# Kernel tuning notes

Hardware: AMD Instinct MI355X
Metric: run time of the kernel (lower is better)

Reference implementation:

```python
import jax, jax.numpy as jnp
import numpy as np

EMB_DIM = 1024
B, T = 32, 2048
N_FLIGHTS = 30
# Action index layout (ActionEnumerator): 0=no_flight, 1=cancel, 2=no_reservation,
# 3..32 = book flight i, 33..62 = change flight i  -> n_actions = 63

def setup_inputs() -> dict:
    key = jax.random.key(0)
    k0, k1, k2, k3, k4 = jax.random.split(key, 5)
    scale = 1.0 / np.sqrt(EMB_DIM)
    return {
        "embs": jax.random.normal(k0, (B, T, EMB_DIM), dtype=jnp.float32),
        "W_status": jax.random.uniform(k1, (5, EMB_DIM), jnp.float32, -scale, scale),
        "b_status": jax.random.uniform(k2, (5,), jnp.float32, -scale, scale),
        "W_flight": jax.random.uniform(k3, (N_FLIGHTS, EMB_DIM), jnp.float32, -scale, scale),
        "b_flight": jax.random.uniform(k4, (N_FLIGHTS,), jnp.float32, -scale, scale),
    }

def reference(embs, W_status, b_status, W_flight, b_flight):
    # Two small linear heads + softmax
    status_probs = jax.nn.softmax(jnp.einsum('bte,se->bts', embs, W_status) + b_status, axis=-1)
    flight_probs = jax.nn.softmax(jnp.einsum('bte,fe->btf', embs, W_flight) + b_flight, axis=-1)
    no_flight = status_probs[:, :, 0:1]
    no_reservation = status_probs[:, :, 1:2]
    cancel = status_probs[:, :, 2:3]
    change = status_probs[:, :, 3:4]
    book = status_probs[:, :, 4:5]
    # Fused version of the 30-iteration scatter loop: one concat of outer products.
    final_probs = jnp.concatenate(
        [no_flight, cancel, no_reservation,
         book * flight_probs,     # [B,T,30] book flight i
         change * flight_probs],  # [B,T,30] change flight i
        axis=-1)  # [B, T, 63]
    return final_probs
```

## Files before the change

kernel.cpp:

```cpp
#include <hip/hip_runtime.h>
#include <math.h>


typedef __bf16 bf16x8 __attribute__((ext_vector_type(8)));
typedef float  f32x4  __attribute__((ext_vector_type(4)));

#define ROWS_PER_BLOCK 256
#define KSTEPS   32
#define HALF_KS  16

__global__ __launch_bounds__(1024, 4)
void fused_heads_kernel(const float* __restrict__ embs,
                        const float* __restrict__ W_status,
                        const float* __restrict__ b_status,
                        const float* __restrict__ W_flight,
                        const float* __restrict__ b_flight,
                        float* __restrict__ out) {
    __shared__ bf16x8 Bsh[HALF_KS * 3 * 64];

    const int tid  = threadIdx.x;
    const int lane = tid & 63;
    const int wv   = tid >> 6;
    const int n    = lane & 15;
    const int q    = lane >> 4;

    const int rowbase = blockIdx.x * ROWS_PER_BLOCK + wv * 16;
    const float* aptr = embs + (size_t)(rowbase + n) * 1024 + q * 8;

    f32x4 acc0 = {0.f, 0.f, 0.f, 0.f};
    f32x4 acc1 = {0.f, 0.f, 0.f, 0.f};
    f32x4 acc2 = {0.f, 0.f, 0.f, 0.f};

    float4 ca0 = *(const float4*)(aptr);
    float4 ca1 = *(const float4*)(aptr + 4);

    for (int half = 0; half < 2; ++half) {
        __syncthreads();

#pragma unroll
        for (int i = 0; i < 3; ++i) {
            const int d   = tid + i * 1024;
            const int L   = d & 63;
            const int ksf = d >> 6;
            const int ksl = ksf / 3;
            const int f   = ksf - ksl * 3;
            const int bn  = f * 16 + (L & 15);
            const int bk  = (half * HALF_KS + ksl) * 32 + (L >> 4) * 8;
            bf16x8 w;
#pragma unroll
            for (int j = 0; j < 8; ++j) w[j] = (__bf16)0.0f;
            if (bn < 35) {
                const float* src = (bn < 5) ? (W_status + bn * 1024 + bk)
                                            : (W_flight + (bn - 5) * 1024 + bk);
                const float4 w0 = *(const float4*)(src);
                const float4 w1 = *(const float4*)(src + 4);
                w[0] = (__bf16)w0.x; w[1] = (__bf16)w0.y;
                w[2] = (__bf16)w0.z; w[3] = (__bf16)w0.w;
                w[4] = (__bf16)w1.x; w[5] = (__bf16)w1.y;
                w[6] = (__bf16)w1.z; w[7] = (__bf16)w1.w;
            }
            Bsh[d] = w;
        }
        __syncthreads();

#pragma unroll 4
        for (int kl = 0; kl < HALF_KS; ++kl) {
            const int ks  = half * HALF_KS + kl;
            const int nks = (ks < KSTEPS - 1) ? ks + 1 : ks;
            const float4 na0 = *(const float4*)(aptr + nks * 32);
            const float4 na1 = *(const float4*)(aptr + nks * 32 + 4);

            bf16x8 af;
            af[0] = (__bf16)ca0.x; af[1] = (__bf16)ca0.y;
            af[2] = (__bf16)ca0.z; af[3] = (__bf16)ca0.w;
            af[4] = (__bf16)ca1.x; af[5] = (__bf16)ca1.y;
            af[6] = (__bf16)ca1.z; af[7] = (__bf16)ca1.w;

            const bf16x8 b0 = Bsh[(kl * 3 + 0) * 64 + lane];
            const bf16x8 b1 = Bsh[(kl * 3 + 1) * 64 + lane];
            const bf16x8 b2 = Bsh[(kl * 3 + 2) * 64 + lane];

            acc0 = __builtin_amdgcn_mfma_f32_16x16x32_bf16(af, b0, acc0, 0, 0, 0);
            acc1 = __builtin_amdgcn_mfma_f32_16x16x32_bf16(af, b1, acc1, 0, 0, 0);
            acc2 = __builtin_amdgcn_mfma_f32_16x16x32_bf16(af, b2, acc2, 0, 0, 0);

            ca0 = na0; ca1 = na1;
        }
    }

    const float bias0 = (n < 5) ? b_status[n] : b_flight[n - 5];
    const float bias1 = b_flight[n + 11];
    const float bias2 = (n < 3) ? b_flight[n + 27] : 0.0f;
    const int   gb    = lane & 48;

#pragma unroll
    for (int i = 0; i < 4; ++i) {
        const float v0 = acc0[i] + bias0;
        const float v1 = acc1[i] + bias1;
        const float v2 = (n < 3) ? (acc2[i] + bias2) : -INFINITY;

        float ms = (n < 5) ? v0 : -INFINITY;
        float mf = fmaxf((n >= 5) ? v0 : -INFINITY, fmaxf(v1, v2));
#pragma unroll
        for (int m = 1; m < 16; m <<= 1) {
            ms = fmaxf(ms, __shfl_xor(ms, m));
            mf = fmaxf(mf, __shfl_xor(mf, m));
        }

        const float es  = (n < 5)  ? __expf(v0 - ms) : 0.0f;
        const float ef0 = (n >= 5) ? __expf(v0 - mf) : 0.0f;
        const float ef1 = __expf(v1 - mf);
        const float ef2 = (n < 3)  ? __expf(v2 - mf) : 0.0f;

        float ss = es;
        float sf = ef0 + ef1 + ef2;
#pragma unroll
        for (int m = 1; m < 16; m <<= 1) {
            ss += __shfl_xor(ss, m);
            sf += __shfl_xor(sf, m);
        }
        const float invs = 1.0f / ss;
        const float invf = 1.0f / sf;

        const float book   = __shfl(es, gb + 4) * invs * invf;
        const float change = __shfl(es, gb + 3) * invs * invf;

        float* orow = out + (size_t)(rowbase + q * 4 + i) * 63;
        if (n == 0) orow[0] = es * invs;
        if (n == 2) orow[1] = es * invs;
        if (n == 1) orow[2] = es * invs;
        if (n >= 5) {
            orow[3 + (n - 5)]  = book   * ef0;
            orow[33 + (n - 5)] = change * ef0;
        }
        orow[3 + (n + 11)]  = book   * ef1;
        orow[33 + (n + 11)] = change * ef1;
        if (n < 3) {
            orow[3 + (n + 27)]  = book   * ef2;
            orow[33 + (n + 27)] = change * ef2;
        }
    }
}

extern "C" void kernel_launch(void* const* d_in, const int* in_sizes, int n_in,
                              void* d_out, int out_size, void* d_ws, size_t ws_size,
                              hipStream_t stream) {
    const float* embs     = (const float*)d_in[0];
    const float* W_status = (const float*)d_in[1];
    const float* b_status = (const float*)d_in[2];
    const float* W_flight = (const float*)d_in[3];
    const float* b_flight = (const float*)d_in[4];
    float* out = (float*)d_out;

    const int rows = in_sizes[0] / 1024;
    const int grid = rows / ROWS_PER_BLOCK;

    fused_heads_kernel<<<grid, 1024, 0, stream>>>(
        embs, W_status, b_status, W_flight, b_flight, out);
}
```

Measured before the change: 391.2 us.

## Stagger K-traversal order per wave and block, load two K-steps per iteration

Each wave now walks the K dimension in pairs of steps, starting at an offset derived from its wave id and block id, and blocks alternate which half of K they process first. The intent is to spread concurrent global reads across different address ranges and channels so they do not hit the same addresses at once. Each iteration also fetches 64 contiguous floats per lane (two K-steps), which puts more loads in flight. The costs are extra register pressure and more complex index arithmetic. A leftover dead code block is also present.

```diff
diff --git a/kernel.cpp b/kernel.cpp
--- a/kernel.cpp
+++ b/kernel.cpp
@@ -6,8 +6,9 @@
 typedef float  f32x4  __attribute__((ext_vector_type(4)));
 
 #define ROWS_PER_BLOCK 256
-#define KSTEPS   32
-#define HALF_KS  16
+#define KSTEPS    32
+#define HALF_KS   16
+#define HALF_PAIRS 8
 
 __global__ __launch_bounds__(1024, 4)
 void fused_heads_kernel(const float* __restrict__ embs,
@@ -27,14 +28,26 @@
     const int rowbase = blockIdx.x * ROWS_PER_BLOCK + wv * 16;
     const float* aptr = embs + (size_t)(rowbase + n) * 1024 + q * 8;
 
+    const int proffs = (wv + (int)blockIdx.x * 3) & 7;
+    const int h0     = (int)blockIdx.x & 1;
+
     f32x4 acc0 = {0.f, 0.f, 0.f, 0.f};
     f32x4 acc1 = {0.f, 0.f, 0.f, 0.f};
     f32x4 acc2 = {0.f, 0.f, 0.f, 0.f};
 
-    float4 ca0 = *(const float4*)(aptr);
-    float4 ca1 = *(const float4*)(aptr + 4);
+    {
+        const int gp0 = h0 * HALF_PAIRS + proffs;
+        const float* p0 = aptr + gp0 * 64;
+        (void)p0;
+    }
+    const float* pf0 = aptr + (h0 * HALF_PAIRS + proffs) * 64;
+    float4 ca0 = *(const float4*)(pf0);
+    float4 ca1 = *(const float4*)(pf0 + 4);
+    float4 ca2 = *(const float4*)(pf0 + 32);
+    float4 ca3 = *(const float4*)(pf0 + 36);
 
-    for (int half = 0; half < 2; ++half) {
+    for (int ph = 0; ph < 2; ++ph) {
+        const int h = h0 ^ ph;
         __syncthreads();
 
 #pragma unroll
@@ -45,7 +58,7 @@
             const int ksl = ksf / 3;
             const int f   = ksf - ksl * 3;
             const int bn  = f * 16 + (L & 15);
-            const int bk  = (half * HALF_KS + ksl) * 32 + (L >> 4) * 8;
+            const int bk  = (h * HALF_KS + ksl) * 32 + (L >> 4) * 8;
             bf16x8 w;
 #pragma unroll
             for (int j = 0; j < 8; ++j) w[j] = (__bf16)0.0f;
@@ -64,27 +77,41 @@
         __syncthreads();
 
 #pragma unroll 4
-        for (int kl = 0; kl < HALF_KS; ++kl) {
-            const int ks  = half * HALF_KS + kl;
-            const int nks = (ks < KSTEPS - 1) ? ks + 1 : ks;
-            const float4 na0 = *(const float4*)(aptr + nks * 32);
-            const float4 na1 = *(const float4*)(aptr + nks * 32 + 4);
+        for (int pl = 0; pl < HALF_PAIRS; ++pl) {
+            const int psl = (pl + proffs) & 7;
+            int ngp;
+            if (pl < HALF_PAIRS - 1)  ngp = h * HALF_PAIRS + ((pl + 1 + proffs) & 7);
+            else if (ph == 0)         ngp = (h0 ^ 1) * HALF_PAIRS + proffs;
+            else                      ngp = h * HALF_PAIRS + psl;
+            const float* np = aptr + ngp * 64;
+            const float4 na0 = *(const float4*)(np);
+            const float4 na1 = *(const float4*)(np + 4);
+            const float4 na2 = *(const float4*)(np + 32);
+            const float4 na3 = *(const float4*)(np + 36);
 
-            bf16x8 af;
-            af[0] = (__bf16)ca0.x; af[1] = (__bf16)ca0.y;
-            af[2] = (__bf16)ca0.z; af[3] = (__bf16)ca0.w;
-            af[4] = (__bf16)ca1.x; af[5] = (__bf16)ca1.y;
-            af[6] = (__bf16)ca1.z; af[7] = (__bf16)ca1.w;
+            const bf16x8* bp = &Bsh[(psl * 6) * 64 + lane];
 
-            const bf16x8 b0 = Bsh[(kl * 3 + 0) * 64 + lane];
-            const bf16x8 b1 = Bsh[(kl * 3 + 1) * 64 + lane];
-            const bf16x8 b2 = Bsh[(kl * 3 + 2) * 64 + lane];
+            bf16x8 af0;
+            af0[0] = (__bf16)ca0.x; af0[1] = (__bf16)ca0.y;
+            af0[2] = (__bf16)ca0.z; af0[3] = (__bf16)ca0.w;
+            af0[4] = (__bf16)ca1.x; af0[5] = (__bf16)ca1.y;
+            af0[6] = (__bf16)ca1.z; af0[7] = (__bf16)ca1.w;
 
-            acc0 = __builtin_amdgcn_mfma_f32_16x16x32_bf16(af, b0, acc0, 0, 0, 0);
-            acc1 = __builtin_amdgcn_mfma_f32_16x16x32_bf16(af, b1, acc1, 0, 0, 0);
-            acc2 = __builtin_amdgcn_mfma_f32_16x16x32_bf16(af, b2, acc2, 0, 0, 0);
+            acc0 = __builtin_amdgcn_mfma_f32_16x16x32_bf16(af0, bp[0],   acc0, 0, 0, 0);
+            acc1 = __builtin_amdgcn_mfma_f32_16x16x32_bf16(af0, bp[64],  acc1, 0, 0, 0);
+            acc2 = __builtin_amdgcn_mfma_f32_16x16x32_bf16(af0, bp[128], acc2, 0, 0, 0);
 
-            ca0 = na0; ca1 = na1;
+            bf16x8 af1;
+            af1[0] = (__bf16)ca2.x; af1[1] = (__bf16)ca2.y;
+            af1[2] = (__bf16)ca2.z; af1[3] = (__bf16)ca2.w;
+            af1[4] = (__bf16)ca3.x; af1[5] = (__bf16)ca3.y;
+            af1[6] = (__bf16)ca3.z; af1[7] = (__bf16)ca3.w;
+
+            acc0 = __builtin_amdgcn_mfma_f32_16x16x32_bf16(af1, bp[192], acc0, 0, 0, 0);
+            acc1 = __builtin_amdgcn_mfma_f32_16x16x32_bf16(af1, bp[256], acc1, 0, 0, 0);
+            acc2 = __builtin_amdgcn_mfma_f32_16x16x32_bf16(af1, bp[320], acc2, 0, 0, 0);
+
+            ca0 = na0; ca1 = na1; ca2 = na2; ca3 = na3;
         }
     }
 
```

After: 373.0 us. -4.7%, faster.
